# Performance work log

Hardware: AMD Instinct MI355X
Metric: run time of the kernel (lower is better)

## Reference

```python
import jax, jax.numpy as jnp
import numpy as np

B, N, C_SA, OUT = 16, 2048, 512, 1024
BN_EPS = 1e-5


def pconv(x, w, b=None):
    # 1x1 Conv1d: x [B,Cin,N], w [Cout,Cin] -> [B,Cout,N]
    y = jnp.einsum('oc,bcn->bon', w, x)
    return y if b is None else y + b[None, :, None]


def setup_inputs() -> dict:
    key = jax.random.key(0)
    ks = jax.random.split(key, 16)
    s = lambda k, shape: jax.random.normal(k, shape, dtype=jnp.float32) * 0.05
    return {
        'x': jax.random.normal(ks[0], (B, 3, N), dtype=jnp.float32),
        'w1': s(ks[1], (128, 21)), 'b1': s(ks[2], (128,)),
        'w2': s(ks[3], (256, 128)), 'b2': s(ks[4], (256,)),
        'w3': s(ks[5], (512, 512)), 'b3': s(ks[6], (512,)),
        'w4': s(ks[7], (OUT, 512)), 'b4': s(ks[8], (OUT,)),
        'wqk': s(ks[9], (C_SA // 4, C_SA)),            # q_conv.weight tied to k_conv.weight, no bias
        'wv': s(ks[10], (C_SA, C_SA)), 'bv': s(ks[11], (C_SA,)),
        'wt': s(ks[12], (C_SA, C_SA)), 'bt': s(ks[13], (C_SA,)),
        'gamma': jnp.ones((C_SA,), dtype=jnp.float32),
        'beta': jnp.zeros((C_SA,), dtype=jnp.float32),
    }


def reference(x, w1, b1, w2, b2, w3, b3, w4, b4, wqk, wv, bv, wt, bt, gamma, beta):
    b, _, n = x.shape
    # positional encoding on [B,N,3]: [t, sin(t*2^i), cos(t*2^i)] for i in 0..2 -> 21 channels
    t = jnp.transpose(x, (0, 2, 1))
    enc = [t]
    for f in (1.0, 2.0, 4.0):
        enc.append(jnp.sin(t * f))
        enc.append(jnp.cos(t * f))
    h = jnp.transpose(jnp.concatenate(enc, axis=-1), (0, 2, 1))  # [B,21,N]

    h = jax.nn.relu(pconv(h, w1, b1))               # [B,128,N]
    h = pconv(h, w2, b2)                            # [B,256,N]
    g = jnp.max(h, axis=2)                          # [B,256]
    h = jnp.concatenate([h, jnp.broadcast_to(g[:, :, None], (b, g.shape[1], n))], axis=1)  # [B,512,N]
    h = jax.nn.relu(pconv(h, w3, b3))               # [B,512,N]

    # SA_Layer (offset attention, double normalization)
    xq = jnp.einsum('oc,bcn->bno', wqk, h)          # [B,N,128]
    xk = jnp.einsum('oc,bcn->bon', wqk, h)          # [B,128,N]
    xv = pconv(h, wv, bv)                           # [B,512,N]
    energy = jnp.einsum('bqo,bok->bqk', xq, xk)     # [B,N,N]
    attn = jax.nn.softmax(energy, axis=-1)
    attn = attn / (1e-9 + jnp.sum(attn, axis=1, keepdims=True))  # L1 renorm over query dim
    x_r = jnp.einsum('bck,bqk->bcq', xv, attn)      # x_v @ attn^T -> [B,512,N]
    d = pconv(h - x_r, wt, bt)
    # BatchNorm1d, training mode (batch statistics, biased variance)
    mu = jnp.mean(d, axis=(0, 2))
    var = jnp.var(d, axis=(0, 2))
    d = gamma[None, :, None] * (d - mu[None, :, None]) * jax.lax.rsqrt(var + BN_EPS)[None, :, None] + beta[None, :, None]
    h = h + jax.nn.relu(d)

    h = pconv(h, w4, b4)                            # [B,OUT,N]
    return jnp.max(h, axis=2)                       # [B,OUT]
```

## Files before the change

### kernel.cpp

```cpp
#include <hip/hip_runtime.h>
#include <cmath>

#define GN 2048
#define GB 16

typedef __attribute__((ext_vector_type(8))) short bf8_t;
typedef __attribute__((ext_vector_type(4))) float f4_t;

__device__ __forceinline__ short f2bf(float f) {
    union { float f; unsigned u; } v; v.f = f;
    unsigned r = v.u + 0x7FFFu + ((v.u >> 16) & 1u);
    return (short)(r >> 16);
}
__device__ __forceinline__ float bf2f(short s) {
    union { unsigned u; float f; } v; v.u = ((unsigned)(unsigned short)s) << 16;
    return v.f;
}

__device__ __forceinline__ void load16_lds(const short* g, short* l) {
    __builtin_amdgcn_global_load_lds(
        (const __attribute__((address_space(1))) unsigned int*)g,
        (__attribute__((address_space(3))) unsigned int*)l, 16, 0, 0);
}

__device__ __forceinline__ float wave_max(float v) {
#pragma unroll
    for (int o = 32; o > 0; o >>= 1) v = fmaxf(v, __shfl_xor(v, o, 64));
    return v;
}
__device__ __forceinline__ float block_max(float v) {
    __shared__ float sm[4];
    v = wave_max(v);
    if ((threadIdx.x & 63) == 0) sm[threadIdx.x >> 6] = v;
    __syncthreads();
    v = fmaxf(fmaxf(sm[0], sm[1]), fmaxf(sm[2], sm[3]));
    __syncthreads();
    return v;
}

__global__ __launch_bounds__(256) void f2b_k(const float* __restrict__ s,
                                             short* __restrict__ d, int n) {
    int i = blockIdx.x * 256 + threadIdx.x;
    if (i < n) d[i] = f2bf(s[i]);
}

__global__ __launch_bounds__(256) void posenc_conv1_k(
    const float* __restrict__ x, const float* __restrict__ w1,
    const float* __restrict__ b1, short* __restrict__ h1) {
    __shared__ float w[128 * 21];
    __shared__ float bb[128];
    __shared__ float se[256][21];
    const int tid = threadIdx.x;
    for (int i = tid; i < 128 * 21; i += 256) w[i] = w1[i];
    if (tid < 128) bb[tid] = b1[tid];
    int p0 = blockIdx.x * 256;
    int p = p0 + tid, b = p >> 11, n = p & (GN - 1);
    const float* xb = x + (long)b * 3 * GN + n;
    float t0 = xb[0], t1 = xb[GN], t2 = xb[2 * GN];
    se[tid][0] = t0; se[tid][1] = t1; se[tid][2] = t2;
    se[tid][3] = sinf(t0); se[tid][4] = sinf(t1); se[tid][5] = sinf(t2);
    se[tid][6] = cosf(t0); se[tid][7] = cosf(t1); se[tid][8] = cosf(t2);
    se[tid][9] = sinf(2.f * t0); se[tid][10] = sinf(2.f * t1); se[tid][11] = sinf(2.f * t2);
    se[tid][12] = cosf(2.f * t0); se[tid][13] = cosf(2.f * t1); se[tid][14] = cosf(2.f * t2);
    se[tid][15] = sinf(4.f * t0); se[tid][16] = sinf(4.f * t1); se[tid][17] = sinf(4.f * t2);
    se[tid][18] = cosf(4.f * t0); se[tid][19] = cosf(4.f * t1); se[tid][20] = cosf(4.f * t2);
    __syncthreads();
    short* outb = h1 + (long)p0 * 128;
    for (int it = 0; it < 128; ++it) {
        int L = it * 256 + tid;
        int pl = L >> 7, o = L & 127;
        float s = bb[o];
        const float* er = se[pl];
        const float* wr = &w[o * 21];
#pragma unroll
        for (int c = 0; c < 21; ++c) s = fmaf(wr[c], er[c], s);
        outb[L] = f2bf(fmaxf(s, 0.f));
    }
}

template <int MODE, int BIAS, bool RELU>
__global__ __launch_bounds__(256) void mm_k(
    const short* __restrict__ A, int lda, long long aB,
    const short* __restrict__ B, int ldb, long long bB,
    const float* __restrict__ bias, int biasStride,
    const short* __restrict__ aux, long long auxB,
    const float* __restrict__ rsv,
    float* __restrict__ Cf, long long cfB,
    short* __restrict__ Cb, long long cbB,
    float* __restrict__ Pmax,
    int ldc, int K) {
    const int z = blockIdx.z;
    A += (long long)z * aB;
    B += (long long)z * bB;
    if (MODE == 4) { aux += (long long)z * auxB; rsv += (long long)z * GN; }
    if (MODE == 1) Cf += (long long)z * cfB;
    if (MODE == 2 || MODE == 4 || MODE == 6) Cb += (long long)z * cbB;
    if (MODE == 6) Pmax += (long long)z * GN * 32;
    const int row0 = blockIdx.x * 128, col0 = blockIdx.y * 128;
    const int tid = threadIdx.x;
    const int lane = tid & 63, w = tid >> 6;
    const int r = lane & 15, q = lane >> 4;
    const int wr = w >> 1, wc = w & 1;

    __shared__ short lA[4096];
    __shared__ short lB[4096];

    f4_t acc[4][4] = {};

    const int sRow = lane >> 2;
    const int sKb = (lane & 3) ^ ((lane >> 3) & 3);
    const long aG = (long)(row0 + w * 32 + sRow) * lda + sKb * 8;
    const long bG = (long)(col0 + w * 32 + sRow) * ldb + sKb * 8;
    short* ldsA0 = lA + (w * 32) * 32;
    short* ldsA1 = lA + (w * 32 + 16) * 32;
    short* ldsB0 = lB + (w * 32) * 32;
    short* ldsB1 = lB + (w * 32 + 16) * 32;

    const int sw = (q ^ ((r >> 1) & 3)) * 8;
    int aoff[4], boff[4];
#pragma unroll
    for (int i = 0; i < 4; ++i) {
        aoff[i] = (wr * 64 + i * 16 + r) * 32 + sw;
        boff[i] = (wc * 64 + i * 16 + r) * 32 + sw;
    }

    for (int k0 = 0; k0 < K; k0 += 32) {
        __syncthreads();
        load16_lds(A + aG + k0, ldsA0);
        load16_lds(A + aG + (long)16 * lda + k0, ldsA1);
        load16_lds(B + bG + k0, ldsB0);
        load16_lds(B + bG + (long)16 * ldb + k0, ldsB1);
        asm volatile("s_waitcnt vmcnt(0)" ::: "memory");
        __syncthreads();
        bf8_t av[4], bv[4];
#pragma unroll
        for (int i = 0; i < 4; ++i) av[i] = *(const bf8_t*)(lA + aoff[i]);
#pragma unroll
        for (int j = 0; j < 4; ++j) bv[j] = *(const bf8_t*)(lB + boff[j]);
#pragma unroll
        for (int i = 0; i < 4; ++i)
#pragma unroll
            for (int j = 0; j < 4; ++j)
                acc[i][j] = __builtin_amdgcn_mfma_f32_16x16x32_bf16(av[i], bv[j], acc[i][j], 0, 0, 0);
    }

    if constexpr (MODE == 5) {
        int b = row0 >> 11;
        int rw = (blockIdx.x * 2 + wr) & 31;
#pragma unroll
        for (int j = 0; j < 4; ++j) {
            float vm = -1e30f;
#pragma unroll
            for (int i = 0; i < 4; ++i)
#pragma unroll
                for (int e = 0; e < 4; ++e) vm = fmaxf(vm, acc[i][j][e]);
            vm = fmaxf(vm, __shfl_xor(vm, 16, 64));
            vm = fmaxf(vm, __shfl_xor(vm, 32, 64));
            if (q == 0) {
                int gcol = col0 + wc * 64 + j * 16 + r;
                Pmax[(((long)b * 1024 + gcol) << 5) + rw] = vm + bias[gcol];
            }
        }
    } else if constexpr (MODE == 6) {
        float rsum[4][4] = {};
#pragma unroll
        for (int j = 0; j < 4; ++j) {
            int gcol = col0 + wc * 64 + j * 16 + r;
#pragma unroll
            for (int i = 0; i < 4; ++i) {
#pragma unroll
                for (int e = 0; e < 4; ++e) {
                    int grow = row0 + wr * 64 + i * 16 + q * 4 + e;
                    float ex = __expf(acc[i][j][e]);
                    rsum[i][e] += ex;
                    Cb[(long)grow * ldc + gcol] = f2bf(ex);
                }
            }
        }
#pragma unroll
        for (int i = 0; i < 4; ++i)
#pragma unroll
            for (int e = 0; e < 4; ++e) {
                float v = rsum[i][e];
                v += __shfl_xor(v, 1, 64);
                v += __shfl_xor(v, 2, 64);
                v += __shfl_xor(v, 4, 64);
                v += __shfl_xor(v, 8, 64);
                if (r == 0) {
                    int grow = row0 + wr * 64 + i * 16 + q * 4 + e;
                    Pmax[((long)grow << 5) + blockIdx.y * 2 + wc] = v;
                }
            }
    } else if constexpr (MODE == 4) {
#pragma unroll
        for (int i = 0; i < 4; ++i) {
#pragma unroll
            for (int e = 0; e < 4; ++e) {
                int grow = row0 + wr * 64 + i * 16 + q * 4 + e;
                float rsr = rsv[grow];
                long ob = (long)grow * ldc + col0 + wc * 64 + r;
#pragma unroll
                for (int j = 0; j < 4; ++j) {
                    long off = ob + j * 16;
                    Cb[off] = f2bf(bf2f(aux[off]) - acc[i][j][e] * rsr);
                }
            }
        }
    } else {
        const int b2d = (BIAS == 3) ? (row0 >> 11) : 0;
#pragma unroll
        for (int j = 0; j < 4; ++j) {
            int gcol = col0 + wc * 64 + j * 16 + r;
            float bvv = 0.f;
            if constexpr (BIAS == 1) bvv = bias[gcol];
            if constexpr (BIAS == 3) bvv = bias[b2d * biasStride + gcol];
#pragma unroll
            for (int i = 0; i < 4; ++i) {
#pragma unroll
                for (int e = 0; e < 4; ++e) {
                    int grow = row0 + wr * 64 + i * 16 + q * 4 + e;
                    float v = acc[i][j][e] + bvv;
                    if constexpr (BIAS == 2) v += bias[grow];
                    if constexpr (RELU) v = fmaxf(v, 0.f);
                    long off = (long)grow * ldc + gcol;
                    if constexpr (MODE == 1) Cf[off] = v;
                    if constexpr (MODE == 2) Cb[off] = f2bf(v);
                }
            }
        }
    }
}

__global__ __launch_bounds__(256) void rs_k(const float* __restrict__ rp,
                                            float* __restrict__ rs) {
    int i = blockIdx.x * 256 + threadIdx.x;
    const float* p = rp + ((long)i << 5);
    float s = 0.f;
#pragma unroll
    for (int j = 0; j < 32; ++j) s += p[j];
    rs[i] = 1.f / s;
}

__global__ __launch_bounds__(256) void maxn1_k(const short* __restrict__ h2,
                                               float* __restrict__ gp) {
    int b = blockIdx.x, s = blockIdx.y, c = threadIdx.x;
    const short* p = h2 + ((long)b * GN + s * 128) * 256 + c;
    float m = -1e30f;
    for (int n = 0; n < 128; ++n) m = fmaxf(m, bf2f(p[(long)n * 256]));
    gp[((b * 16 + s) << 8) + c] = m;
}
__global__ __launch_bounds__(256) void maxn2_k(const float* __restrict__ gp,
                                               float* __restrict__ g) {
    int b = blockIdx.x, c = threadIdx.x;
    float m = -1e30f;
    for (int s = 0; s < 16; ++s) m = fmaxf(m, gp[((b * 16 + s) << 8) + c]);
    g[(b << 8) + c] = m;
}

__global__ __launch_bounds__(256) void cvec_k(const float* __restrict__ w3,
                                              const float* __restrict__ b3,
                                              const float* __restrict__ g,
                                              float* __restrict__ cvec) {
    int idx = blockIdx.x * 256 + threadIdx.x;
    int b = idx >> 9, o = idx & 511;
    const float* gb = g + (b << 8);
    const float* wr = w3 + (long)o * 512 + 256;
    float s = b3[o];
    for (int c = 0; c < 256; ++c) s = fmaf(wr[c], gb[c], s);
    cvec[idx] = s;
}

__global__ __launch_bounds__(256) void colsum1_k(const short* __restrict__ Ab,
                                                 const float* __restrict__ rs,
                                                 float* __restrict__ cp) {
    int kb = blockIdx.x, qs = blockIdx.y, z = blockIdx.z;
    int k = kb * 256 + threadIdx.x;
    const short* p = Ab + (long)z * GN * GN + (long)qs * 64 * GN + k;
    const float* rv = rs + z * GN + qs * 64;
    float s = 0.f;
    for (int qq = 0; qq < 64; ++qq) s += bf2f(p[(long)qq * GN]) * rv[qq];
    cp[((z * 32 + qs) * GN) + k] = s;
}
__global__ __launch_bounds__(256) void colsum2_k(const float* __restrict__ cp,
                                                 float* __restrict__ cs) {
    int k = blockIdx.x * 256 + threadIdx.x, z = blockIdx.y;
    float s = 1e-9f;
    for (int qs = 0; qs < 32; ++qs) s += cp[((z * 32 + qs) * GN) + k];
    cs[z * GN + k] = s;
}

__global__ __launch_bounds__(256) void xvscale_k(short* __restrict__ xvc,
                                                 const float* __restrict__ cs) {
    long idx = ((long)blockIdx.x * 256 + threadIdx.x) * 4;
    int p = (int)(idx & 32767);
    short* ptr = xvc + idx;
    float4 cv = *(const float4*)(cs + p);
    uint2 u = *(const uint2*)ptr;
    short* sp = (short*)&u;
    sp[0] = f2bf(bf2f(sp[0]) / cv.x);
    sp[1] = f2bf(bf2f(sp[1]) / cv.y);
    sp[2] = f2bf(bf2f(sp[2]) / cv.z);
    sp[3] = f2bf(bf2f(sp[3]) / cv.w);
    *(uint2*)ptr = u;
}

__global__ __launch_bounds__(256) void bn1_k(const short* __restrict__ d,
                                             float* __restrict__ bs1,
                                             float* __restrict__ bs2) {
    int s = blockIdx.x, t = threadIdx.x;
    const short* p = d + (long)s * 256 * 512 + t * 2;
    float s0 = 0.f, q0 = 0.f, s1 = 0.f, q1 = 0.f;
    for (int rr = 0; rr < 256; ++rr) {
        unsigned int u = *(const unsigned int*)(p + (long)rr * 512);
        float v0 = bf2f((short)(u & 0xffffu));
        float v1 = bf2f((short)(u >> 16));
        s0 += v0; q0 = fmaf(v0, v0, q0);
        s1 += v1; q1 = fmaf(v1, v1, q1);
    }
    bs1[s * 512 + t * 2] = s0; bs1[s * 512 + t * 2 + 1] = s1;
    bs2[s * 512 + t * 2] = q0; bs2[s * 512 + t * 2 + 1] = q1;
}
__global__ __launch_bounds__(256) void bn2_k(const float* __restrict__ bs1,
                                             const float* __restrict__ bs2,
                                             const float* __restrict__ gamma,
                                             const float* __restrict__ beta,
                                             float* __restrict__ sc,
                                             float* __restrict__ sh) {
    int c = blockIdx.x * 256 + threadIdx.x;
    float s = 0.f, s2 = 0.f;
    for (int i = 0; i < 128; ++i) {
        s += bs1[i * 512 + c];
        s2 += bs2[i * 512 + c];
    }
    const float cnt = (float)(GB * GN);
    float mu = s / cnt;
    float var = s2 / cnt - mu * mu;
    float r = rsqrtf(var + 1e-5f);
    float gm = gamma[c] * r;
    sc[c] = gm;
    sh[c] = beta[c] - gm * mu;
}

__global__ __launch_bounds__(256) void bn_apply_k(const short* __restrict__ h3b,
                                                  const short* __restrict__ d,
                                                  const float* __restrict__ sc,
                                                  const float* __restrict__ sh,
                                                  short* __restrict__ h4) {
    long bidx = ((long)blockIdx.x * 256 + threadIdx.x) * 4;
    int c = (int)(bidx & 511);
    uint2 du = *(const uint2*)(d + bidx);
    short* ds = (short*)&du;
    uint2 hu = *(const uint2*)(h3b + bidx);
    short* hs = (short*)&hu;
    float4 a4 = *(const float4*)(sc + c);
    float4 b4 = *(const float4*)(sh + c);
    float r0 = bf2f(hs[0]) + fmaxf(fmaf(bf2f(ds[0]), a4.x, b4.x), 0.f);
    float r1 = bf2f(hs[1]) + fmaxf(fmaf(bf2f(ds[1]), a4.y, b4.y), 0.f);
    float r2 = bf2f(hs[2]) + fmaxf(fmaf(bf2f(ds[2]), a4.z, b4.z), 0.f);
    float r3 = bf2f(hs[3]) + fmaxf(fmaf(bf2f(ds[3]), a4.w, b4.w), 0.f);
    uint2 o;
    o.x = (unsigned short)f2bf(r0) | ((unsigned)(unsigned short)f2bf(r1) << 16);
    o.y = (unsigned short)f2bf(r2) | ((unsigned)(unsigned short)f2bf(r3) << 16);
    *(uint2*)(h4 + bidx) = o;
}

__global__ __launch_bounds__(256) void max_final_k(const float* __restrict__ P,
                                                   float* __restrict__ out) {
    int i = blockIdx.x * 256 + threadIdx.x;
    const float* p = P + ((long)i << 5);
    float m = p[0];
#pragma unroll
    for (int j = 1; j < 32; ++j) m = fmaxf(m, p[j]);
    out[i] = m;
}

extern "C" void kernel_launch(void* const* d_in, const int* in_sizes, int n_in,
                              void* d_out, int out_size, void* d_ws, size_t ws_size,
                              hipStream_t stream) {
    const float* x = (const float*)d_in[0];
    const float* w1 = (const float*)d_in[1];
    const float* b1 = (const float*)d_in[2];
    const float* w2 = (const float*)d_in[3];
    const float* b2 = (const float*)d_in[4];
    const float* w3 = (const float*)d_in[5];
    const float* b3 = (const float*)d_in[6];
    const float* w4 = (const float*)d_in[7];
    const float* b4 = (const float*)d_in[8];
    const float* wqk = (const float*)d_in[9];
    const float* wv = (const float*)d_in[10];
    const float* bv = (const float*)d_in[11];
    const float* wt = (const float*)d_in[12];
    const float* bt = (const float*)d_in[13];
    const float* gamma = (const float*)d_in[14];
    const float* beta = (const float*)d_in[15];
    float* out = (float*)d_out;

    char* base = (char*)d_ws;
    short* h3b = (short*)base;
    short* hsT = (short*)(base + 33554432);
    short* kT  = (short*)(base + 67108864);
    short* xvc = (short*)(base + 75497472);
    short* EA  = (short*)(base + 109051904);
    short* h1T = (short*)(base + 109051904);
    short* h2T = (short*)(base + 117440512);
    short* dTb = (short*)(base + 109051904);
    short* h4T = (short*)(base + 67108864);
    char* S = base + 243269632;
    float* gp   = (float*)(S);
    float* g    = (float*)(S + 262144);
    float* cvec = (float*)(S + 278528);
    float* cp   = (float*)(S + 311296);
    float* rp   = cp;
    float* cs   = (float*)(S + 4505600);
    float* bs1  = (float*)(S + 4636672);
    float* bs2  = (float*)(S + 4898816);
    float* bnsc = (float*)(S + 5160960);
    float* bnsh = (float*)(S + 5163008);
    float* Pmax = (float*)(S + 5165056);
    short* w2b  = (short*)(S + 7262208);
    short* w3b  = (short*)(S + 7327744);
    short* wqkb = (short*)(S + 7852032);
    short* wvb  = (short*)(S + 7983104);
    short* wtb  = (short*)(S + 8507392);
    short* w4b  = (short*)(S + 9031680);
    float* rs   = (float*)(S + 10080256);

    f2b_k<<<128, 256, 0, stream>>>(w2, w2b, 256 * 128);
    f2b_k<<<1024, 256, 0, stream>>>(w3, w3b, 512 * 512);
    f2b_k<<<256, 256, 0, stream>>>(wqk, wqkb, 128 * 512);
    f2b_k<<<1024, 256, 0, stream>>>(wv, wvb, 512 * 512);
    f2b_k<<<1024, 256, 0, stream>>>(wt, wtb, 512 * 512);
    f2b_k<<<2048, 256, 0, stream>>>(w4, w4b, 1024 * 512);

    posenc_conv1_k<<<128, 256, 0, stream>>>(x, w1, b1, h1T);

    mm_k<2, 1, false><<<dim3(256, 2, 1), 256, 0, stream>>>(
        h1T, 128, 0, w2b, 128, 0, b2, 0, nullptr, 0, nullptr,
        nullptr, 0, h2T, 0, nullptr, 256, 128);

    maxn1_k<<<dim3(GB, 16), 256, 0, stream>>>(h2T, gp);
    maxn2_k<<<GB, 256, 0, stream>>>(gp, g);

    cvec_k<<<32, 256, 0, stream>>>(w3, b3, g, cvec);

    mm_k<2, 3, true><<<dim3(256, 4, 1), 256, 0, stream>>>(
        h2T, 256, 0, w3b, 512, 0, cvec, 512, nullptr, 0, nullptr,
        nullptr, 0, h3b, 0, nullptr, 512, 256);

    mm_k<2, 0, false><<<dim3(256, 1, 1), 256, 0, stream>>>(
        h3b, 512, 0, wqkb, 512, 0, nullptr, 0, nullptr, 0, nullptr,
        nullptr, 0, kT, 0, nullptr, 128, 512);

    mm_k<2, 2, false><<<dim3(4, 256, 1), 256, 0, stream>>>(
        wvb, 512, 0, h3b, 512, 0, bv, 0, nullptr, 0, nullptr,
        nullptr, 0, xvc, 0, nullptr, 32768, 512);

    mm_k<6, 0, false><<<dim3(16, 16, 16), 256, 0, stream>>>(
        kT, 128, (long long)GN * 128, kT, 128, (long long)GN * 128,
        nullptr, 0, nullptr, 0, nullptr, nullptr, 0,
        EA, (long long)GN * GN, rp, GN, 128);
    rs_k<<<128, 256, 0, stream>>>(rp, rs);
    colsum1_k<<<dim3(8, 32, GB), 256, 0, stream>>>(EA, rs, cp);
    colsum2_k<<<dim3(8, GB), 256, 0, stream>>>(cp, cs);
    xvscale_k<<<16384, 256, 0, stream>>>(xvc, cs);
    mm_k<4, 0, false><<<dim3(16, 4, 16), 256, 0, stream>>>(
        EA, GN, (long long)GN * GN,
        xvc, 32768, (long long)GN,
        nullptr, 0,
        h3b, (long long)GN * 512, rs,
        nullptr, 0,
        hsT, (long long)GN * 512,
        nullptr, 512, GN);

    mm_k<2, 1, false><<<dim3(256, 4, 1), 256, 0, stream>>>(
        hsT, 512, 0, wtb, 512, 0, bt, 0, nullptr, 0, nullptr,
        nullptr, 0, dTb, 0, nullptr, 512, 512);

    bn1_k<<<128, 256, 0, stream>>>(dTb, bs1, bs2);
    bn2_k<<<2, 256, 0, stream>>>(bs1, bs2, gamma, beta, bnsc, bnsh);

    bn_apply_k<<<16384, 256, 0, stream>>>(h3b, dTb, bnsc, bnsh, h4T);

    mm_k<5, 1, false><<<dim3(256, 8, 1), 256, 0, stream>>>(
        h4T, 512, 0, w4b, 512, 0, b4, 0, nullptr, 0, nullptr,
        nullptr, 0, nullptr, 0, Pmax, 1024, 512);

    max_final_k<<<64, 256, 0, stream>>>(Pmax, out);
}
```

Before: 565.7 us.

## Double-buffer LDS tiles to overlap global loads with MFMA compute

Shared-memory tiles for A and B are doubled so the next K-slice is fetched into the alternate buffer while the current one feeds the MFMAs. The old loop synchronised twice per iteration and waited for each load before computing; the new loop has one wait and barrier per step. This uses twice the LDS per block, which may lower occupancy, and the overlap is limited because the code still waits on vmcnt(0) each iteration.

```diff
diff --git a/kernel.cpp b/kernel.cpp
--- a/kernel.cpp
+++ b/kernel.cpp
@@ -102,8 +102,8 @@
     const int r = lane & 15, q = lane >> 4;
     const int wr = w >> 1, wc = w & 1;
 
-    __shared__ short lA[4096];
-    __shared__ short lB[4096];
+    __shared__ short lA[8192];
+    __shared__ short lB[8192];
 
     f4_t acc[4][4] = {};
 
@@ -111,10 +111,6 @@
     const int sKb = (lane & 3) ^ ((lane >> 3) & 3);
     const long aG = (long)(row0 + w * 32 + sRow) * lda + sKb * 8;
     const long bG = (long)(col0 + w * 32 + sRow) * ldb + sKb * 8;
-    short* ldsA0 = lA + (w * 32) * 32;
-    short* ldsA1 = lA + (w * 32 + 16) * 32;
-    short* ldsB0 = lB + (w * 32) * 32;
-    short* ldsB1 = lB + (w * 32 + 16) * 32;
 
     const int sw = (q ^ ((r >> 1) & 3)) * 8;
     int aoff[4], boff[4];
@@ -124,24 +120,41 @@
         boff[i] = (wc * 64 + i * 16 + r) * 32 + sw;
     }
 
-    for (int k0 = 0; k0 < K; k0 += 32) {
-        __syncthreads();
-        load16_lds(A + aG + k0, ldsA0);
-        load16_lds(A + aG + (long)16 * lda + k0, ldsA1);
-        load16_lds(B + bG + k0, ldsB0);
-        load16_lds(B + bG + (long)16 * ldb + k0, ldsB1);
-        asm volatile("s_waitcnt vmcnt(0)" ::: "memory");
-        __syncthreads();
+    auto stage = [&](int k0, int buf) {
+        short* a = lA + buf * 4096 + (w * 32) * 32;
+        short* b = lB + buf * 4096 + (w * 32) * 32;
+        load16_lds(A + aG + k0, a);
+        load16_lds(A + aG + (long)16 * lda + k0, a + 512);
+        load16_lds(B + bG + k0, b);
+        load16_lds(B + bG + (long)16 * ldb + k0, b + 512);
+    };
+    auto compute = [&](int buf) {
+        const short* la = lA + buf * 4096;
+        const short* lb = lB + buf * 4096;
         bf8_t av[4], bv[4];
 #pragma unroll
-        for (int i = 0; i < 4; ++i) av[i] = *(const bf8_t*)(lA + aoff[i]);
-#pragma unroll
-        for (int j = 0; j < 4; ++j) bv[j] = *(const bf8_t*)(lB + boff[j]);
+        for (int i = 0; i < 4; ++i) av[i] = *(const bf8_t*)(la + aoff[i]);
+#pragma unroll
+        for (int j = 0; j < 4; ++j) bv[j] = *(const bf8_t*)(lb + boff[j]);
 #pragma unroll
         for (int i = 0; i < 4; ++i)
 #pragma unroll
             for (int j = 0; j < 4; ++j)
                 acc[i][j] = __builtin_amdgcn_mfma_f32_16x16x32_bf16(av[i], bv[j], acc[i][j], 0, 0, 0);
+    };
+
+    stage(0, 0);
+    asm volatile("s_waitcnt vmcnt(0)" ::: "memory");
+    __syncthreads();
+    int buf = 0;
+    for (int k0 = 0; k0 < K; k0 += 32) {
+        if (k0 + 32 < K) stage(k0 + 32, buf ^ 1);
+        compute(buf);
+        if (k0 + 32 < K) {
+            asm volatile("s_waitcnt vmcnt(0)" ::: "memory");
+            __syncthreads();
+        }
+        buf ^= 1;
     }
 
     if constexpr (MODE == 5) {
```

Measured after the change: 629.9 us. 11.3% more time.
